# Optimization experiments

Measured on AMD Instinct MI355X. Metric: run time of the kernel, lower is better.

## Reference

```python
import jax, jax.numpy as jnp
import numpy as np

R_CUTOFF = 5.0
BASIS = 8
NMAX = 8
NSPECIES = 3
EMBED = 16


def _chebyshev_basis(r, r_cutoff, basis_size):
    fc = jnp.where(r < r_cutoff, 0.5 * jnp.cos(jnp.pi * r / r_cutoff) + 0.5, 0.0)
    x = 2.0 * (r / r_cutoff) ** 2 - 1.0
    polys = [jnp.ones_like(x), x]
    for n in range(2, basis_size):
        polys.append(2.0 * x * polys[-1] - polys[-2])
    basis = jnp.stack(polys[:basis_size], axis=-1)  # [E, basis]
    return 0.5 * (basis + 1.0) * fc[:, None]


def setup_inputs() -> dict:
    key = jax.random.key(0)
    ks = jax.random.split(key, 12)
    N, K = 20000, 32
    E = N * K
    positions = jax.random.normal(ks[0], (N, 3), dtype=jnp.float32)
    species = jax.random.randint(ks[1], (N,), 0, NSPECIES, dtype=jnp.int32)
    magmoms = jax.random.normal(ks[2], (N, 3), dtype=jnp.float32)
    # i-major edge list: exactly K edges per atom, grouped by center atom.
    i_idx = jnp.repeat(jnp.arange(N, dtype=jnp.int32), K)
    j_idx = jax.random.randint(ks[3], (E,), 0, N, dtype=jnp.int32)
    edge_index = jnp.stack([i_idx, j_idx], axis=0)
    shifts = jnp.zeros((E, 3), dtype=jnp.float32)
    rb_coefficients = 0.1 * jax.random.normal(ks[4], (NSPECIES * NSPECIES, NMAX, BASIS), dtype=jnp.float32)
    species_embedding = 0.1 * jax.random.normal(ks[5], (NSPECIES, EMBED), dtype=jnp.float32)
    struct_dim = NMAX + NMAX * (NMAX + 1)  # 80
    mag_dim = 3 + 7 * NMAX + 3 * NMAX * NMAX  # 251
    return {
        'positions': positions, 'species': species, 'magmoms': magmoms,
        'edge_index': edge_index, 'shifts': shifts,
        'rb_coefficients': rb_coefficients, 'species_embedding': species_embedding,
        'struct_shift': jnp.zeros(struct_dim, jnp.float32),
        'struct_scale': jnp.ones(struct_dim, jnp.float32),
        'mag_shift': jnp.zeros(mag_dim, jnp.float32),
        'mag_scale': jnp.ones(mag_dim, jnp.float32),
        'atomic_energy_shift': 0.1 * jax.random.normal(ks[6], (NSPECIES,), dtype=jnp.float32),
        'w_struct': 0.05 * jax.random.normal(ks[7], (EMBED + struct_dim,), dtype=jnp.float32),
        'b_struct': 0.05 * jax.random.normal(ks[8], (1,), dtype=jnp.float32),
        'w_mag': 0.05 * jax.random.normal(ks[9], (EMBED + mag_dim,), dtype=jnp.float32),
        'b_mag': 0.05 * jax.random.normal(ks[10], (1,), dtype=jnp.float32),
    }


def _forward(positions, magmoms, shifts, rb_coefficients, species_embedding,
             struct_shift, struct_scale, mag_shift, mag_scale, atomic_energy_shift,
             w_struct, b_struct, w_mag, b_mag, species, edge_index):
    N = positions.shape[0]
    E = edge_index.shape[1]
    K = E // N  # regular neighbor count (edge list is i-major)
    i_idx, j_idx = edge_index[0], edge_index[1]
    r_ij = positions[j_idx] - positions[i_idx] + shifts          # [E,3]
    dist = jnp.linalg.norm(r_ij, axis=-1)                        # [E]
    f_k = _chebyshev_basis(dist, R_CUTOFF, BASIS)                # [E,basis]
    pair_idx = species[i_idx] * NSPECIES + species[j_idx]
    phi = jnp.einsum('enk,ek->en', rb_coefficients[pair_idx], f_k)  # [E,n]
    seg = lambda x: jax.ops.segment_sum(x, i_idx, num_segments=N)
    d = jnp.maximum(dist, 1e-8)[:, None]
    r_hat = r_ij / d
    # --- structural descriptors ---
    d_radial = seg(phi)                                          # [N,n]
    P = seg(phi[:, :, None] * r_hat[:, None, :])                 # [N,n,3]
    PP = jnp.einsum('ina,ima->inm', P, P)
    tu = np.triu_indices(NMAX)
    d_ang_l1 = PP[:, tu[0], tu[1]]
    eye3 = jnp.eye(3, dtype=r_ij.dtype)
    traceless = r_hat[:, :, None] * r_hat[:, None, :] - eye3 / 3.0  # [E,3,3]
    Q = seg(phi[:, :, None, None] * traceless[:, None, :, :])       # [N,n,3,3]
    Qf = Q.reshape(N, NMAX, 9)
    QQ = jnp.einsum('ina,ima->inm', Qf, Qf)
    d_ang_l2 = QQ[:, tu[0], tu[1]]
    desc_struct = jnp.concatenate([d_radial, d_ang_l1, d_ang_l2], axis=-1)
    # --- magnetic descriptors ---
    u = jnp.sum(magmoms * magmoms, axis=-1)                      # [N]
    m_norm = jnp.linalg.norm(magmoms, axis=-1, keepdims=True)
    m_dir = jnp.where(m_norm > 1e-8, magmoms / jnp.maximum(m_norm, 1e-8), 0.0)
    M = seg(phi[:, :, None] * m_dir[j_idx][:, None, :])          # [N,n,3]
    # A_{nm}(i) = sum_{a<b within atom i's edge block} phi_n(a) phi_m(b) (r_a x r_b)
    phi_g = phi.reshape(N, K, NMAX)
    r_g = r_ij.reshape(N, K, 3)
    cross = jnp.cross(r_g[:, :, None, :], r_g[:, None, :, :])    # [N,K,K,3]
    mask = jnp.triu(jnp.ones((K, K), dtype=phi.dtype), k=1)
    tmp = jnp.einsum('iabd,ab,ibm->iamd', cross, mask, phi_g)    # [N,K,3,n]
    A = jnp.einsum('ian,iamd->inmd', phi_g, tmp)                 # [N,n,n,3]
    d_amp = jnp.stack([u, u ** 2, u ** 3], axis=-1)
    d_iso = jnp.sum(m_dir[:, None, :] * M, axis=-1)              # [N,n]
    Qm = jnp.einsum('anij,aj->ani', Q, m_dir)
    d_sia = jnp.sum(m_dir[:, None, :] * Qm, axis=-1)
    mQ = jnp.einsum('ai,amij->amj', m_dir, Q)
    d_sae = jnp.einsum('amj,anj->amn', mQ, M).reshape(N, -1)
    m_cross_M = jnp.cross(jnp.broadcast_to(m_dir[:, None, :], M.shape), M)
    d_dmi = jnp.einsum('inmd,imd->inm', A, m_cross_M).reshape(N, -1)
    u_col = u[:, None]
    d_amp_mix = jnp.concatenate([u_col * d_iso, u_col * d_sia, u_col * d_dmi], axis=-1)
    u_j = u[j_idx]
    d_nbr_amp = seg(phi * u_j[:, None])
    W = seg(phi[:, :, None] * (u_j[:, None] * m_dir[j_idx])[:, None, :])
    d_nbr_amp_ex = jnp.sum(m_dir[:, None, :] * W, axis=-1)
    d_nbr_amp_ex_mix = u_col * d_nbr_amp_ex
    desc_mag = jnp.concatenate([d_amp, d_iso, d_sia, d_sae, d_dmi, d_amp_mix,
                                d_nbr_amp, d_nbr_amp_ex, d_nbr_amp_ex_mix], axis=-1)
    # --- scaling + linear readout heads + per-species shift ---
    ds = (desc_struct - struct_shift) / struct_scale
    dm = (desc_mag - mag_shift) / mag_scale
    emb = species_embedding[species]
    e_struct = jnp.concatenate([emb, ds], axis=-1) @ w_struct + b_struct[0]
    e_mag = jnp.concatenate([emb, dm], axis=-1) @ w_mag + b_mag[0]
    return e_struct + e_mag + atomic_energy_shift[species]        # [N]


def reference(positions, species, magmoms, edge_index, shifts, rb_coefficients,
              species_embedding, struct_shift, struct_scale, mag_shift, mag_scale,
              atomic_energy_shift, w_struct, b_struct, w_mag, b_mag):
    return _forward(positions, magmoms, shifts, rb_coefficients, species_embedding,
                    struct_shift, struct_scale, mag_shift, mag_scale, atomic_energy_shift,
                    w_struct, b_struct, w_mag, b_mag, species, edge_index)
```

## Files before the change

### kernel.cpp

```cpp
#include <hip/hip_runtime.h>

#define NSPEC  3
#define EMBEDD 16
#define KMAX   32
#define RCUT   5.0f
#define PADR   36

typedef float v2f __attribute__((ext_vector_type(2)));

__constant__ int TUN[36] = {0,0,0,0,0,0,0,0, 1,1,1,1,1,1,1, 2,2,2,2,2,2, 3,3,3,3,3, 4,4,4,4, 5,5,5, 6,6, 7};
__constant__ int TUM[36] = {0,1,2,3,4,5,6,7, 1,2,3,4,5,6,7, 2,3,4,5,6,7, 3,4,5,6,7, 4,5,6,7, 5,6,7, 6,7, 7};


template<int CTRL, int RMASK, bool BC>
__device__ __forceinline__ float dpp_mov0(float x) {
    return __int_as_float(__builtin_amdgcn_update_dpp(
        0, __float_as_int(x), CTRL, RMASK, 0xF, BC));
}
__device__ __forceinline__ float prefix32(float x) {
    x += dpp_mov0<0x111, 0xF, true >(x);
    x += dpp_mov0<0x112, 0xF, true >(x);
    x += dpp_mov0<0x114, 0xF, true >(x);
    x += dpp_mov0<0x118, 0xF, true >(x);
    x += dpp_mov0<0x142, 0xA, false>(x);
    return x;
}
__device__ __forceinline__ float swz_xor16(float x) {
    return __int_as_float(__builtin_amdgcn_ds_swizzle(__float_as_int(x), 0x401F));
}
__device__ __forceinline__ float red_k4(float x) {
    x += dpp_mov0<0x128, 0xF, true>(x);
    x += swz_xor16(x);
    return x;
}
__device__ __forceinline__ v2f red_k4_v2(v2f v) {
    v2f t;
    t.x = dpp_mov0<0x128, 0xF, true>(v.x);
    t.y = dpp_mov0<0x128, 0xF, true>(v.y);
    v += t;
    t.x = swz_xor16(v.x);
    t.y = swz_xor16(v.y);
    v += t;
    return v;
}
__device__ __forceinline__ float red32(float x) {
    x += dpp_mov0<0x121, 0xF, true>(x);
    x += dpp_mov0<0x122, 0xF, true>(x);
    x += dpp_mov0<0x124, 0xF, true>(x);
    x += dpp_mov0<0x128, 0xF, true>(x);
    x += swz_xor16(x);
    return x;
}
__device__ __forceinline__ void lds_fence() {
    asm volatile("s_waitcnt lgkmcnt(0)" ::: "memory");
}

struct __align__(16) AtomLds {
    float phiT[8 * PADR];
    float rhx[KMAX], rhy[KMAX], rhz[KMAX];
    float mdx[KMAX], mdy[KMAX], mdz[KMAX];
    float uj[KMAX];
    float P4[8*4];
    float Q8[8*8];
    float M4[8*4];
    float mQ4[8*4];
    float wv4[8*4];
};

__global__ __launch_bounds__(256)
void magpot_setup(const float* __restrict__ sshift, const float* __restrict__ sscale,
                  const float* __restrict__ mshift, const float* __restrict__ mscale,
                  const float* __restrict__ wstruct, const float* __restrict__ bstruct,
                  const float* __restrict__ wmag, const float* __restrict__ bmag,
                  float* __restrict__ ws)
{
    __shared__ float red[4];
    const int t = threadIdx.x;
    float c = 0.0f;
    for (int idx = t; idx < 80; idx += 256) {
        const float w = wstruct[16 + idx] / sscale[idx];
        ws[idx] = w;
        c += w * sshift[idx];
    }
    for (int idx = t; idx < 251; idx += 256) {
        const float w = wmag[16 + idx] / mscale[idx];
        ws[80 + idx] = w;
        c += w * mshift[idx];
    }
    if (t < EMBEDD) ws[332 + t] = wstruct[t] + wmag[t];
    if (t < 64) {
        ws[400 + t] = wmag[16 + 83 + t]  / mscale[83 + t];
        ws[464 + t] = wmag[16 + 163 + t] / mscale[163 + t];
    }
    #pragma unroll
    for (int d = 1; d <= 32; d <<= 1) c += __shfl_xor(c, d, 64);
    if ((t & 63) == 0) red[t >> 6] = c;
    __syncthreads();
    if (t == 0) ws[331] = bstruct[0] + bmag[0] - (red[0] + red[1] + red[2] + red[3]);
}

__global__ __launch_bounds__(256)
void magpot_main(const float* __restrict__ pos,
                 const int*   __restrict__ species,
                 const float* __restrict__ mag,
                 const int*   __restrict__ eidx,
                 const float* __restrict__ shifts,
                 const float* __restrict__ rb,
                 const float* __restrict__ semb,
                 const float* __restrict__ aes,
                 const float* __restrict__ ws,
                 float* __restrict__ out,
                 int N, int E, int K)
{
    __shared__ AtomLds lds[8];

    const int lane64 = threadIdx.x & 63;
    const int wv     = threadIdx.x >> 6;
    const int h      = lane64 >> 5;
    const int s      = lane64 & 31;
    const int ea     = 31 - s;
    const int i      = blockIdx.x * 8 + wv * 2 + h;
    const bool valid = (i < N);
    const int isafe  = valid ? i : 0;
    AtomLds& L = lds[wv * 2 + h];

    const float* wm = ws + 80;

    const int   spi = species[isafe];
    const float mgx = mag[3*isafe+0], mgy = mag[3*isafe+1], mgz = mag[3*isafe+2];
    const float u_i = mgx*mgx + mgy*mgy + mgz*mgz;
    const float mi_inv = (u_i > 1e-16f) ? __builtin_amdgcn_rsqf(u_i) : 0.0f;
    const float mix = mgx*mi_inv, miy = mgy*mi_inv, miz = mgz*mi_inv;
    const float pix = pos[3*isafe+0], piy = pos[3*isafe+1], piz = pos[3*isafe+2];

    float phi[8];
    float rx = 0.0f, ry = 0.0f, rz = 0.0f;
    #pragma unroll
    for (int n = 0; n < 8; ++n) phi[n] = 0.0f;

    if (ea < K) {
        const int e = isafe * K + ea;
        const int j = eidx[E + e];
        rx = pos[3*j+0] - pix + shifts[3*e+0];
        ry = pos[3*j+1] - piy + shifts[3*e+1];
        rz = pos[3*j+2] - piz + shifts[3*e+2];
        const float d2 = rx*rx + ry*ry + rz*rz;
        const float dist = __builtin_amdgcn_sqrtf(d2);
        const float fc = (dist < RCUT)
            ? (0.5f * __builtin_amdgcn_cosf(dist * 0.1f) + 0.5f)
            : 0.0f;
        const float xr = dist * (1.0f/RCUT);
        const float x  = 2.0f * xr * xr - 1.0f;
        v2f f2[4];
        {
            float fp[8];
            float Tm2 = 1.0f, Tm1 = x;
            fp[0] = 0.5f * (Tm2 + 1.0f) * fc;
            fp[1] = 0.5f * (Tm1 + 1.0f) * fc;
            #pragma unroll
            for (int k = 2; k < 8; ++k) {
                const float T = 2.0f * x * Tm1 - Tm2;
                Tm2 = Tm1; Tm1 = T;
                fp[k] = 0.5f * (T + 1.0f) * fc;
            }
            f2[0] = (v2f){fp[0], fp[1]};
            f2[1] = (v2f){fp[2], fp[3]};
            f2[2] = (v2f){fp[4], fp[5]};
            f2[3] = (v2f){fp[6], fp[7]};
        }
        const int spj = species[j];
        const float4* rb4 = (const float4*)(rb + (spi * NSPEC + spj) * 64);
        #pragma unroll
        for (int n = 0; n < 8; ++n) {
            const float4 r0 = rb4[n*2+0];
            const float4 r1 = rb4[n*2+1];
            v2f a2 = f2[0] * (v2f){r0.x, r0.y};
            a2 += f2[1] * (v2f){r0.z, r0.w};
            a2 += f2[2] * (v2f){r1.x, r1.y};
            a2 += f2[3] * (v2f){r1.z, r1.w};
            const float ph = a2.x + a2.y;
            phi[n] = ph;
            L.phiT[n*PADR + ea] = ph;
        }
        const float dinv = (dist > 1e-8f) ? __builtin_amdgcn_rcpf(dist) : 1e8f;
        L.rhx[ea] = rx * dinv;
        L.rhy[ea] = ry * dinv;
        L.rhz[ea] = rz * dinv;
        const float mjx = mag[3*j+0], mjy = mag[3*j+1], mjz = mag[3*j+2];
        const float uj = mjx*mjx + mjy*mjy + mjz*mjz;
        const float mjinv = (uj > 1e-16f) ? __builtin_amdgcn_rsqf(uj) : 0.0f;
        L.mdx[ea] = mjx * mjinv;
        L.mdy[ea] = mjy * mjinv;
        L.mdz[ea] = mjz * mjinv;
        L.uj[ea] = uj;
    } else {
        #pragma unroll
        for (int n = 0; n < 8; ++n) L.phiT[n*PADR + ea] = 0.0f;
        L.rhx[ea] = 0.0f; L.rhy[ea] = 0.0f; L.rhz[ea] = 0.0f;
        L.mdx[ea] = 0.0f; L.mdy[ea] = 0.0f; L.mdz[ea] = 0.0f;
        L.uj[ea] = 0.0f;
    }
    lds_fence();

    float p = 0.0f;

    {
        const int k4 = s >> 3;
        const int n  = s & 7;
        const float4* phR = (const float4*)&L.phiT[n*PADR + k4*8];
        const float4* hxR = (const float4*)&L.rhx[k4*8];
        const float4* hyR = (const float4*)&L.rhy[k4*8];
        const float4* hzR = (const float4*)&L.rhz[k4*8];
        const float4* dxR = (const float4*)&L.mdx[k4*8];
        const float4* dyR = (const float4*)&L.mdy[k4*8];
        const float4* dzR = (const float4*)&L.mdz[k4*8];
        const float4* ujR = (const float4*)&L.uj[k4*8];

        float s_dr = 0.0f, sP2 = 0.0f, s_nb = 0.0f, sM2 = 0.0f, sW0 = 0.0f;
        v2f A1 = {0,0};
        v2f A3 = {0,0};
        v2f A4 = {0,0};
        v2f A5 = {0,0};
        v2f A6 = {0,0};
        v2f A8 = {0,0};

        auto acc = [&](float ph, float hx, float hy, float hz,
                       float dx, float dy, float dz, float uj) {
            const float phu = ph * uj;
            s_dr += ph;
            s_nb += phu;
            sP2 += ph * hz;
            sM2 += ph * dz;
            sW0 += phu * dx;
            A1 += ph * (v2f){hx, hy};
            A3 += ph * ((v2f){hx, hx} * (v2f){hx, hy});
            A4 += ph * ((v2f){hx, hy} * (v2f){hz, hy});
            A5 += ph * ((v2f){hy, hz} * (v2f){hz, hz});
            A6 += ph * (v2f){dx, dy};
            A8 += phu * (v2f){dy, dz};
        };
        #pragma unroll
        for (int q = 0; q < 2; ++q) {
            const float4 ph4 = phR[q], hx4 = hxR[q], hy4 = hyR[q], hz4 = hzR[q];
            const float4 dx4 = dxR[q], dy4 = dyR[q], dz4 = dzR[q], uj4 = ujR[q];
            acc(ph4.x, hx4.x, hy4.x, hz4.x, dx4.x, dy4.x, dz4.x, uj4.x);
            acc(ph4.y, hx4.y, hy4.y, hz4.y, dx4.y, dy4.y, dz4.y, uj4.y);
            acc(ph4.z, hx4.z, hy4.z, hz4.z, dx4.z, dy4.z, dz4.z, uj4.z);
            acc(ph4.w, hx4.w, hy4.w, hz4.w, dx4.w, dy4.w, dz4.w, uj4.w);
        }
        s_dr = red_k4(s_dr); sP2 = red_k4(sP2); s_nb = red_k4(s_nb);
        sM2 = red_k4(sM2);   sW0 = red_k4(sW0);
        A1 = red_k4_v2(A1); A3 = red_k4_v2(A3); A4 = red_k4_v2(A4);
        A5 = red_k4_v2(A5); A6 = red_k4_v2(A6); A8 = red_k4_v2(A8);

        if (k4 == 0) {
            const float dr3 = s_dr * (1.0f/3.0f);
            const float aP0 = A1.x, aP1 = A1.y, aP2 = sP2;
            const float aQ0 = A3.x - dr3, aQ1 = A3.y, aQ2 = A4.x;
            const float aQ3 = A4.y - dr3, aQ4 = A5.x, aQ5 = A5.y - dr3;
            const float aM0 = A6.x, aM1 = A6.y, aM2 = sM2;
            const float aW0 = sW0, aW1 = A8.x, aW2 = A8.y;

            ((float4*)L.P4)[n]     = make_float4(aP0, aP1, aP2, 0.0f);
            ((float4*)L.Q8)[2*n]   = make_float4(aQ0, aQ1, aQ2, aQ3);
            ((float4*)L.Q8)[2*n+1] = make_float4(aQ4, aQ5, 0.0f, 0.0f);
            ((float4*)L.M4)[n]     = make_float4(aM0, aM1, aM2, 0.0f);
            const float mq0 = aQ0*mix + aQ1*miy + aQ2*miz;
            const float mq1 = aQ1*mix + aQ3*miy + aQ4*miz;
            const float mq2 = aQ2*mix + aQ4*miy + aQ5*miz;
            ((float4*)L.mQ4)[n]    = make_float4(mq0, mq1, mq2, 0.0f);
            ((float4*)L.wv4)[n]    = make_float4(miy*aM2 - miz*aM1,
                                                 miz*aM0 - mix*aM2,
                                                 mix*aM1 - miy*aM0, 0.0f);
            const float diso = mix*aM0 + miy*aM1 + miz*aM2;
            const float dsia = mq0*mix + mq1*miy + mq2*miz;
            const float dnex = mix*aW0 + miy*aW1 + miz*aW2;
            p += s_dr * ws[n] + s_nb * wm[227 + n]
               + diso * wm[3 + n]  + dsia * wm[11 + n]  + dnex * wm[235 + n]
               + u_i * (diso * wm[147 + n] + dsia * wm[155 + n] + dnex * wm[243 + n]);
        }
        if (s == 8) {
            const float u2 = u_i * u_i;
            p += u_i * wm[0] + u2 * wm[1] + u2 * u_i * wm[2];
        }
        if (s < EMBEDD)
            p += semb[spi * EMBEDD + s] * ws[332 + s];
    }
    lds_fence();

    {
        const v2f* cw1 = (const v2f*)(ws + 400);
        const v2f* cw2 = (const v2f*)(ws + 464);
        v2f B1[4] = {{0,0},{0,0},{0,0},{0,0}};
        v2f B2[4] = {{0,0},{0,0},{0,0},{0,0}};
        #pragma unroll
        for (int n = 0; n < 8; ++n) {
            #pragma unroll
            for (int jj = 0; jj < 4; ++jj) {
                B1[jj] += phi[n] * cw1[n*4 + jj];
                B2[jj] += phi[n] * cw2[n*4 + jj];
            }
        }
        v2f Bp[4];
        #pragma unroll
        for (int jj = 0; jj < 4; ++jj) Bp[jj] = B1[jj] + u_i * B2[jj];

        float cdmi = 0.0f;
        #pragma unroll
        for (int m = 0; m < 8; ++m) {
            const float4 wvm = ((const float4*)L.wv4)[m];
            const float vx = phi[m] * rx;
            const float vy = phi[m] * ry;
            const float vz = phi[m] * rz;
            const float Sx = prefix32(vx) - vx;
            const float Sy = prefix32(vy) - vy;
            const float Sz = prefix32(vz) - vz;
            const float cx = ry*Sz - rz*Sy;
            const float cy = rz*Sx - rx*Sz;
            const float cz = rx*Sy - ry*Sx;
            const float Bm = (m & 1) ? Bp[m >> 1].y : Bp[m >> 1].x;
            cdmi = fmaf(Bm, cx*wvm.x + cy*wvm.y + cz*wvm.z, cdmi);
        }
        p += cdmi;
    }

    {
        #pragma unroll
        for (int t2 = 0; t2 < 2; ++t2) {
            const int idx = s + t2*32;
            const int m4 = idx >> 3, n4 = idx & 7;
            const float4 mQm = ((const float4*)L.mQ4)[m4];
            const float4 Mn  = ((const float4*)L.M4)[n4];
            p += (mQm.x*Mn.x + mQm.y*Mn.y + mQm.z*Mn.z) * wm[19 + idx];
        }
        #pragma unroll
        for (int t2 = 0; t2 < 2; ++t2) {
            const int idx = s + t2*32;
            if (idx < 36) {
                const int a = TUN[idx], b = TUM[idx];
                const float4 Pa = ((const float4*)L.P4)[a];
                const float4 Pb = ((const float4*)L.P4)[b];
                const float pp = Pa.x*Pb.x + Pa.y*Pb.y + Pa.z*Pb.z;
                const float4 Qa0 = ((const float4*)L.Q8)[2*a], Qa1 = ((const float4*)L.Q8)[2*a+1];
                const float4 Qb0 = ((const float4*)L.Q8)[2*b], Qb1 = ((const float4*)L.Q8)[2*b+1];
                const float qq = Qa0.x*Qb0.x + Qa0.w*Qb0.w + Qa1.y*Qb1.y
                       + 2.0f*(Qa0.y*Qb0.y + Qa0.z*Qb0.z + Qa1.x*Qb1.x);
                p += pp * ws[8 + idx] + qq * ws[44 + idx];
            }
        }
    }

    p = red32(p);
    if (s == 0 && valid)
        out[i] = p + ws[331] + aes[spi];
}

extern "C" void kernel_launch(void* const* d_in, const int* in_sizes, int n_in,
                              void* d_out, int out_size, void* d_ws, size_t ws_size,
                              hipStream_t stream) {
    const float* pos     = (const float*)d_in[0];
    const int*   spc     = (const int*)  d_in[1];
    const float* mg      = (const float*)d_in[2];
    const int*   eidx    = (const int*)  d_in[3];
    const float* shf     = (const float*)d_in[4];
    const float* rb      = (const float*)d_in[5];
    const float* semb    = (const float*)d_in[6];
    const float* sshift  = (const float*)d_in[7];
    const float* sscale  = (const float*)d_in[8];
    const float* mshift  = (const float*)d_in[9];
    const float* mscale  = (const float*)d_in[10];
    const float* aes     = (const float*)d_in[11];
    const float* wstruct = (const float*)d_in[12];
    const float* bstruct = (const float*)d_in[13];
    const float* wmag    = (const float*)d_in[14];
    const float* bmag    = (const float*)d_in[15];
    float* out = (float*)d_out;
    float* ws  = (float*)d_ws;

    const int N = in_sizes[1];
    const int E = in_sizes[3] / 2;
    const int K = E / N;

    hipLaunchKernelGGL(magpot_setup, dim3(1), dim3(256), 0, stream,
                       sshift, sscale, mshift, mscale, wstruct, bstruct, wmag, bmag, ws);
    hipLaunchKernelGGL(magpot_main, dim3((N + 7) / 8), dim3(256), 0, stream,
                       pos, spc, mg, eidx, shf, rb, semb, aes, ws, out, N, E, K);
}
```

Baseline: 120.8 us.

## Pack per-atom position/species and normalized magmom into float4 tables in prep kernel

New measurement: 119.9 us. No clear change (-0.7%).

```diff
diff --git a/kernel.cpp b/kernel.cpp
--- a/kernel.cpp
+++ b/kernel.cpp
@@ -67,12 +67,11 @@
     float wv4[8*4];
 };
 
-__global__ __launch_bounds__(256)
-void magpot_setup(const float* __restrict__ sshift, const float* __restrict__ sscale,
-                  const float* __restrict__ mshift, const float* __restrict__ mscale,
-                  const float* __restrict__ wstruct, const float* __restrict__ bstruct,
-                  const float* __restrict__ wmag, const float* __restrict__ bmag,
-                  float* __restrict__ ws)
+__device__ void do_setup(const float* sshift, const float* sscale,
+                         const float* mshift, const float* mscale,
+                         const float* wstruct, const float* bstruct,
+                         const float* wmag, const float* bmag,
+                         float* ws)
 {
     __shared__ float red[4];
     const int t = threadIdx.x;
@@ -100,10 +99,34 @@
 }
 
 __global__ __launch_bounds__(256)
-void magpot_main(const float* __restrict__ pos,
+void magpot_prep(const float* __restrict__ pos,
                  const int*   __restrict__ species,
                  const float* __restrict__ mag,
-                 const int*   __restrict__ eidx,
+                 const float* __restrict__ sshift, const float* __restrict__ sscale,
+                 const float* __restrict__ mshift, const float* __restrict__ mscale,
+                 const float* __restrict__ wstruct, const float* __restrict__ bstruct,
+                 const float* __restrict__ wmag, const float* __restrict__ bmag,
+                 float* __restrict__ ws,
+                 int N, int nAtomBlocks)
+{
+    if ((int)blockIdx.x == nAtomBlocks) {
+        do_setup(sshift, sscale, mshift, mscale, wstruct, bstruct, wmag, bmag, ws);
+        return;
+    }
+    const int t = blockIdx.x * 256 + threadIdx.x;
+    if (t >= N) return;
+    const float px = pos[3*t+0], py = pos[3*t+1], pz = pos[3*t+2];
+    const float mx = mag[3*t+0], my = mag[3*t+1], mz = mag[3*t+2];
+    const float u = mx*mx + my*my + mz*mz;
+    const float minv = (u > 1e-16f) ? __builtin_amdgcn_rsqf(u) : 0.0f;
+    float4* atabA = (float4*)(ws + 2048);
+    float4* atabB = (float4*)(ws + 2048) + N;
+    atabA[t] = make_float4(px, py, pz, __int_as_float(species[t]));
+    atabB[t] = make_float4(mx*minv, my*minv, mz*minv, u);
+}
+
+__global__ __launch_bounds__(256)
+void magpot_main(const int*   __restrict__ eidx,
                  const float* __restrict__ shifts,
                  const float* __restrict__ rb,
                  const float* __restrict__ semb,
@@ -125,13 +148,15 @@
     AtomLds& L = lds[wv * 2 + h];
 
     const float* wm = ws + 80;
-
-    const int   spi = species[isafe];
-    const float mgx = mag[3*isafe+0], mgy = mag[3*isafe+1], mgz = mag[3*isafe+2];
-    const float u_i = mgx*mgx + mgy*mgy + mgz*mgz;
-    const float mi_inv = (u_i > 1e-16f) ? __builtin_amdgcn_rsqf(u_i) : 0.0f;
-    const float mix = mgx*mi_inv, miy = mgy*mi_inv, miz = mgz*mi_inv;
-    const float pix = pos[3*isafe+0], piy = pos[3*isafe+1], piz = pos[3*isafe+2];
+    const float4* atabA = (const float4*)(ws + 2048);
+    const float4* atabB = atabA + N;
+
+    const float4 Ai = atabA[isafe];
+    const float4 Bi = atabB[isafe];
+    const float pix = Ai.x, piy = Ai.y, piz = Ai.z;
+    const int   spi = __float_as_int(Ai.w);
+    const float mix = Bi.x, miy = Bi.y, miz = Bi.z;
+    const float u_i = Bi.w;
 
     float phi[8];
     float rx = 0.0f, ry = 0.0f, rz = 0.0f;
@@ -141,9 +166,11 @@
     if (ea < K) {
         const int e = isafe * K + ea;
         const int j = eidx[E + e];
-        rx = pos[3*j+0] - pix + shifts[3*e+0];
-        ry = pos[3*j+1] - piy + shifts[3*e+1];
-        rz = pos[3*j+2] - piz + shifts[3*e+2];
+        const float4 Aj = atabA[j];
+        const float4 Bj = atabB[j];
+        rx = Aj.x - pix + shifts[3*e+0];
+        ry = Aj.y - piy + shifts[3*e+1];
+        rz = Aj.z - piz + shifts[3*e+2];
         const float d2 = rx*rx + ry*ry + rz*rz;
         const float dist = __builtin_amdgcn_sqrtf(d2);
         const float fc = (dist < RCUT)
@@ -168,7 +195,7 @@
             f2[2] = (v2f){fp[4], fp[5]};
             f2[3] = (v2f){fp[6], fp[7]};
         }
-        const int spj = species[j];
+        const int spj = __float_as_int(Aj.w);
         const float4* rb4 = (const float4*)(rb + (spi * NSPEC + spj) * 64);
         #pragma unroll
         for (int n = 0; n < 8; ++n) {
@@ -186,13 +213,10 @@
         L.rhx[ea] = rx * dinv;
         L.rhy[ea] = ry * dinv;
         L.rhz[ea] = rz * dinv;
-        const float mjx = mag[3*j+0], mjy = mag[3*j+1], mjz = mag[3*j+2];
-        const float uj = mjx*mjx + mjy*mjy + mjz*mjz;
-        const float mjinv = (uj > 1e-16f) ? __builtin_amdgcn_rsqf(uj) : 0.0f;
-        L.mdx[ea] = mjx * mjinv;
-        L.mdy[ea] = mjy * mjinv;
-        L.mdz[ea] = mjz * mjinv;
-        L.uj[ea] = uj;
+        L.mdx[ea] = Bj.x;
+        L.mdy[ea] = Bj.y;
+        L.mdz[ea] = Bj.z;
+        L.uj[ea]  = Bj.w;
     } else {
         #pragma unroll
         for (int n = 0; n < 8; ++n) L.phiT[n*PADR + ea] = 0.0f;
@@ -381,8 +405,10 @@
     const int E = in_sizes[3] / 2;
     const int K = E / N;
 
-    hipLaunchKernelGGL(magpot_setup, dim3(1), dim3(256), 0, stream,
-                       sshift, sscale, mshift, mscale, wstruct, bstruct, wmag, bmag, ws);
+    const int nAtomBlocks = (N + 255) / 256;
+    hipLaunchKernelGGL(magpot_prep, dim3(nAtomBlocks + 1), dim3(256), 0, stream,
+                       pos, spc, mg, sshift, sscale, mshift, mscale,
+                       wstruct, bstruct, wmag, bmag, ws, N, nAtomBlocks);
     hipLaunchKernelGGL(magpot_main, dim3((N + 7) / 8), dim3(256), 0, stream,
-                       pos, spc, mg, eidx, shf, rb, semb, aes, ws, out, N, E, K);
-}
+                       eidx, shf, rb, semb, aes, ws, out, N, E, K);
+}
```
